# Kernel optimization log

Hardware: AMD Instinct MI355X
Metric: run time of the kernel (lower is better)

Reference implementation:

```python
import jax, jax.numpy as jnp
import numpy as np

E = 16          # num_expert
CAP = 1024


def setup_inputs() -> dict:
    key = jax.random.key(0)
    k1, k2, k3, k4 = jax.random.split(key, 4)
    B, L, D_in, D_out, S = 2, 4096, 1024, 4096, 512
    inp = jax.random.normal(k1, (B, L, D_in), jnp.float32)
    # counts must sum to B*L; use a balanced assignment (tokens pre-sorted by expert)
    fwd_expert_count = jnp.full((E,), (B * L) // E, dtype=jnp.int32)
    weight = jax.random.normal(k2, (E, D_out, D_in), jnp.float32) * (1.0 / np.sqrt(D_in))
    bias = jax.random.normal(k3, (E, D_out), jnp.float32) * 0.02
    components = jax.random.normal(k4, (E, S, D_out), jnp.float32) * (1.0 / np.sqrt(D_out))
    return {"inp": inp, "fwd_expert_count": fwd_expert_count, "weight": weight,
            "bias": bias, "components": components}


def _forward(inp, fwd_expert_count, weight, bias, components):
    flat = inp.reshape(-1, inp.shape[-1])            # [T, D_in]
    T = flat.shape[0]
    n_exp = fwd_expert_count.shape[0]
    counts = fwd_expert_count.astype(jnp.int32)
    # per-token expert id and position within its expert segment (tokens are
    # contiguous per expert, matching fastmoe's dispatch layout)
    expert_ids = jnp.repeat(jnp.arange(n_exp, dtype=jnp.int32), counts,
                            total_repeat_length=T)                    # [T]
    offsets = jnp.concatenate([jnp.zeros((1,), jnp.int32), jnp.cumsum(counts)])
    pos = jnp.arange(T, dtype=jnp.int32) - offsets[expert_ids]        # [T]
    # scatter tokens into a padded [E, CAP, D_in] buffer (static capacity)
    padded = jnp.zeros((n_exp, CAP, flat.shape[-1]), flat.dtype)
    padded = padded.at[expert_ids, pos].set(flat)
    # grouped expert GEMM: y_e = x_e @ W_e^T + b_e  (padded rows never read back)
    y = jnp.einsum('eci,eoi->eco', padded, weight) + bias[:, None, :]  # [E, CAP, D_out]
    # projection onto components (einsum 'nkd,ksd->nks' in padded layout)
    proj = jnp.einsum('ecd,esd->ecs', y, components)                   # [E, CAP, S]
    # gather real tokens back (the upscale_proj branch in the source is dead code:
    # its result is never used in the returned output)
    out = proj[expert_ids, pos]                                        # [T, S]
    return out.reshape(inp.shape[:-1] + (proj.shape[-1],))


def reference(inp, fwd_expert_count, weight, bias, components):
    return _forward(inp, fwd_expert_count, weight, bias, components)
```

## Files before the change

kernel.cpp:

```cpp
#include <hip/hip_runtime.h>


#define NEXP 16
#define TTOK 8192
#define DIN  1024
#define DOUT 4096
#define SDIM 512
#define LDSS 40

typedef short short8 __attribute__((ext_vector_type(8)));
typedef float floatx4 __attribute__((ext_vector_type(4)));
typedef unsigned short ushort_t;

__device__ __forceinline__ ushort_t f2bf(float f) {
    union { float f; unsigned u; } v; v.f = f;
    unsigned r = v.u + 0x7FFFu + ((v.u >> 16) & 1u);
    return (ushort_t)(r >> 16);
}

#define GLL16(g, l) __builtin_amdgcn_global_load_lds( \
    (const __attribute__((address_space(1))) void*)(g), \
    (__attribute__((address_space(3))) void*)(l), 16, 0, 0)

__global__ __launch_bounds__(256)
void cvt_kernel(const float* __restrict__ src, ushort_t* __restrict__ dst, int n8) {
    const int i = blockIdx.x * 256 + threadIdx.x;
    if (i >= n8) return;
    const float4 a = ((const float4*)src)[2 * i];
    const float4 b = ((const float4*)src)[2 * i + 1];
    short8 o;
    o[0] = (short)f2bf(a.x); o[1] = (short)f2bf(a.y);
    o[2] = (short)f2bf(a.z); o[3] = (short)f2bf(a.w);
    o[4] = (short)f2bf(b.x); o[5] = (short)f2bf(b.y);
    o[6] = (short)f2bf(b.z); o[7] = (short)f2bf(b.w);
    ((short8*)dst)[i] = o;
}

template<bool G1>
__global__ __launch_bounds__(512, 2)
void gemm8p(const ushort_t* __restrict__ Ain, const int* __restrict__ counts,
            const ushort_t* __restrict__ Bin, const float* __restrict__ bias,
            ushort_t* __restrict__ Yout, float* __restrict__ Pout) {
    __shared__ __align__(16) ushort_t As[2 * 16384];
    __shared__ __align__(16) ushort_t Bs[2 * 16384];

    int e, mt, nt, kq;
    if constexpr (G1) {
        const int l = ((blockIdx.x & 7) << 6) | (blockIdx.x >> 3);
        e = l >> 5; nt = (l >> 1) & 15; mt = l & 1; kq = 0;
    } else {
        const int l = ((blockIdx.x & 7) << 5) | (blockIdx.x >> 3);
        e = l >> 4; kq = (l >> 2) & 3; nt = (l >> 1) & 1; mt = l & 1;
    }
    const int LDK = G1 ? DIN : DOUT;

    int off = 0;
    for (int i = 0; i < e; ++i) off += counts[i];
    const int cnt = counts[e];

    const int tid = threadIdx.x, wave = tid >> 6, lane = tid & 63;
    const int wm = wave >> 2, wn = wave & 3;
    const int l15 = lane & 15, quad = lane >> 4;

    const int srow  = (wave << 3) + (lane >> 3);
    const int kbase = (G1 ? 0 : (kq << 10)) + (((lane & 7) ^ (lane >> 3)) << 3);

    const ushort_t* Bseg;
    if constexpr (G1) Bseg = Bin + (size_t)e * DOUT * DIN  + ((size_t)(nt << 8)) * DIN;
    else              Bseg = Bin + (size_t)e * SDIM * DOUT + ((size_t)(nt << 8)) * DOUT;
    const int aseg = off + (mt << 8);

    auto stA = [&](int bufe, int q, int kt) {
        int r = aseg + (q << 6) + srow; if (r >= TTOK) r = TTOK - 1;
        GLL16(Ain + (size_t)r * LDK + kbase + (kt << 6),
              As + bufe + (q << 12) + (wave << 9));
    };
    auto stB = [&](int bufe, int q, int kt) {
        GLL16(Bseg + (size_t)((q << 6) + srow) * LDK + kbase + (kt << 6),
              Bs + bufe + (q << 12) + (wave << 9));
    };
    auto rdA = [&](int bufe, int m, int s) -> short8 {
        return *(const short8*)&As[bufe + ((wm << 7) + (m << 4) + l15) * 64
                                   + ((((s << 2) | quad) ^ (lane & 7)) << 3)];
    };
    auto rdB = [&](int bufe, int n, int s) -> short8 {
        return *(const short8*)&Bs[bufe + ((wn << 6) + (n << 4) + l15) * 64
                                   + ((((s << 2) | quad) ^ (lane & 7)) << 3)];
    };

    floatx4 acc[8][4] = {};
    short8 bf[4][2], af0[2], af1[2];

#define RDB_ALL(BUFE) { _Pragma("unroll") \
    for (int n = 0; n < 4; ++n) { bf[n][0] = rdB(BUFE,n,0); bf[n][1] = rdB(BUFE,n,1); } }
#define RDA2(BUFE, M0) { af0[0]=rdA(BUFE,M0,0); af0[1]=rdA(BUFE,M0,1); \
                         af1[0]=rdA(BUFE,(M0)+1,0); af1[1]=rdA(BUFE,(M0)+1,1); }
#define MFMA16(M0) { \
    __builtin_amdgcn_s_setprio(1); \
    _Pragma("unroll") for (int n = 0; n < 4; ++n) { \
      acc[M0][n]     = __builtin_amdgcn_mfma_f32_16x16x32_bf16(af0[0], bf[n][0], acc[M0][n],     0,0,0); \
      acc[M0][n]     = __builtin_amdgcn_mfma_f32_16x16x32_bf16(af0[1], bf[n][1], acc[M0][n],     0,0,0); \
      acc[(M0)+1][n] = __builtin_amdgcn_mfma_f32_16x16x32_bf16(af1[0], bf[n][0], acc[(M0)+1][n], 0,0,0); \
      acc[(M0)+1][n] = __builtin_amdgcn_mfma_f32_16x16x32_bf16(af1[1], bf[n][1], acc[(M0)+1][n], 0,0,0); } \
    __builtin_amdgcn_s_setprio(0); }
#define BAR() __builtin_amdgcn_s_barrier()
#define VMC6() asm volatile("s_waitcnt vmcnt(6)" ::: "memory")

    stA(0,0,0); stA(0,1,0); stA(0,2,0); stA(0,3,0);
    stB(0,0,0); stB(0,1,0); stB(0,2,0); stB(0,3,0);
    stB(16384,0,1); stB(16384,1,1); stB(16384,2,1); stB(16384,3,1);
    stA(16384,0,1); stA(16384,2,1);
    VMC6();
    BAR();

    #pragma unroll 1
    for (int it = 0; it < 8; ++it) {
        const int tn = 2 * it + 1;
        const int t2 = (it < 7) ? 2 * it + 2 : 0;
        const int t3 = (it < 7) ? 2 * it + 3 : 1;

        RDB_ALL(0); RDA2(0, 0);
        stA(16384,1,tn); stA(16384,3,tn);
        BAR(); MFMA16(0); BAR();

        RDA2(0, 2);
        stB(0,0,t2); stB(0,1,t2);
        BAR(); MFMA16(2); BAR();

        RDA2(0, 4);
        stB(0,2,t2); stA(0,0,t2);
        BAR(); MFMA16(4); BAR();

        RDA2(0, 6);
        stB(0,3,t2); stA(0,2,t2);
        VMC6();
        BAR(); MFMA16(6); BAR();

        RDB_ALL(16384); RDA2(16384, 0);
        stA(0,1,t2); stA(0,3,t2);
        BAR(); MFMA16(0); BAR();

        RDA2(16384, 2);
        stB(16384,0,t3); stB(16384,1,t3);
        BAR(); MFMA16(2); BAR();

        RDA2(16384, 4);
        stB(16384,2,t3); stA(16384,0,t3);
        BAR(); MFMA16(4); BAR();

        RDA2(16384, 6);
        stB(16384,3,t3); stA(16384,2,t3);
        VMC6();
        BAR(); MFMA16(6); BAR();
    }
    asm volatile("s_waitcnt vmcnt(0)" ::: "memory");

#undef RDB_ALL
#undef RDA2
#undef MFMA16
#undef BAR
#undef VMC6

    if constexpr (G1) {
        float bv[4];
        #pragma unroll
        for (int n = 0; n < 4; ++n)
            bv[n] = bias[e * DOUT + (nt << 8) + (wn << 6) + (n << 4) + l15];
        #pragma unroll
        for (int m = 0; m < 8; ++m) {
            #pragma unroll
            for (int rg = 0; rg < 4; ++rg) {
                const int trow = (mt << 8) + (wm << 7) + (m << 4) + (quad << 2) + rg;
                if (trow < cnt) {
                    ushort_t* yp = Yout + (size_t)(off + trow) * DOUT + (nt << 8) + (wn << 6);
                    #pragma unroll
                    for (int n = 0; n < 4; ++n)
                        yp[(n << 4) + l15] = f2bf(acc[m][n][rg] + bv[n]);
                }
            }
        }
    } else {
        float* pp = Pout + (size_t)kq * ((size_t)TTOK * SDIM);
        #pragma unroll
        for (int m = 0; m < 8; ++m) {
            #pragma unroll
            for (int rg = 0; rg < 4; ++rg) {
                const int trow = (mt << 8) + (wm << 7) + (m << 4) + (quad << 2) + rg;
                if (trow < cnt) {
                    float* op = pp + (size_t)(off + trow) * SDIM + (nt << 8) + (wn << 6);
                    #pragma unroll
                    for (int n = 0; n < 4; ++n)
                        op[(n << 4) + l15] = acc[m][n][rg];
                }
            }
        }
    }
}

__global__ __launch_bounds__(256)
void reduce4_kernel(const float* __restrict__ P, float* __restrict__ O) {
    const int i = blockIdx.x * 256 + threadIdx.x;
    const size_t S = (size_t)TTOK * SDIM;
    const float4 a = ((const float4*)P)[i];
    const float4 b = ((const float4*)(P + S))[i];
    const float4 c = ((const float4*)(P + 2 * S))[i];
    const float4 d = ((const float4*)(P + 3 * S))[i];
    ((float4*)O)[i] = make_float4(a.x + b.x + c.x + d.x, a.y + b.y + c.y + d.y,
                                  a.z + b.z + c.z + d.z, a.w + b.w + c.w + d.w);
}

__global__ __launch_bounds__(256, 2)
void gemm1_o(const float* __restrict__ X, const int* __restrict__ counts,
             const float* __restrict__ W, const float* __restrict__ bias,
             ushort_t* __restrict__ Y) {
    __shared__ __align__(16) ushort_t As[128 * LDSS];
    __shared__ __align__(16) ushort_t Bs[128 * LDSS];
    const int bid = blockIdx.x;
    const int e = bid >> 7, r_ = bid & 127;
    const int n_tile = r_ >> 2, m_tile = r_ & 3;
    int off = 0;
    for (int i = 0; i < e; ++i) off += counts[i];
    const int cnt = counts[e];
    const int t = threadIdx.x, wave = t >> 6, lane = t & 63;
    const int wm = (wave & 1) << 6, wn = (wave >> 1) << 6;
    const int l15 = lane & 15, quad = lane >> 4;
    const float* Wp = W + (size_t)e * DOUT * DIN + (size_t)(n_tile << 7) * DIN;
    floatx4 acc[4][4] = {};
    const int srow = t >> 3, scol = (t & 7) << 2;
    for (int k0 = 0; k0 < DIN; k0 += 32) {
        #pragma unroll
        for (int p = 0; p < 4; ++p) {
            const int row = srow + (p << 5);
            int grow = off + (m_tile << 7) + row;
            if (grow >= TTOK) grow = 0;
            const float4 v = *(const float4*)(X + (size_t)grow * DIN + k0 + scol);
            unsigned lo = (unsigned)f2bf(v.x) | ((unsigned)f2bf(v.y) << 16);
            unsigned hi = (unsigned)f2bf(v.z) | ((unsigned)f2bf(v.w) << 16);
            *(uint2*)&As[row * LDSS + scol] = make_uint2(lo, hi);
        }
        #pragma unroll
        for (int p = 0; p < 4; ++p) {
            const int row = srow + (p << 5);
            const float4 v = *(const float4*)(Wp + (size_t)row * DIN + k0 + scol);
            unsigned lo = (unsigned)f2bf(v.x) | ((unsigned)f2bf(v.y) << 16);
            unsigned hi = (unsigned)f2bf(v.z) | ((unsigned)f2bf(v.w) << 16);
            *(uint2*)&Bs[row * LDSS + scol] = make_uint2(lo, hi);
        }
        __syncthreads();
        short8 af[4], bfr[4];
        #pragma unroll
        for (int i = 0; i < 4; ++i) {
            af[i]  = *(const short8*)&As[(wm + (i << 4) + l15) * LDSS + (quad << 3)];
            bfr[i] = *(const short8*)&Bs[(wn + (i << 4) + l15) * LDSS + (quad << 3)];
        }
        #pragma unroll
        for (int mi = 0; mi < 4; ++mi)
            #pragma unroll
            for (int ni = 0; ni < 4; ++ni)
                acc[mi][ni] = __builtin_amdgcn_mfma_f32_16x16x32_bf16(
                    af[mi], bfr[ni], acc[mi][ni], 0, 0, 0);
        __syncthreads();
    }
    float bv[4];
    #pragma unroll
    for (int ni = 0; ni < 4; ++ni)
        bv[ni] = bias[e * DOUT + (n_tile << 7) + wn + (ni << 4) + l15];
    #pragma unroll
    for (int mi = 0; mi < 4; ++mi)
        #pragma unroll
        for (int rg = 0; rg < 4; ++rg) {
            const int trow = (m_tile << 7) + wm + (mi << 4) + (quad << 2) + rg;
            if (trow < cnt) {
                ushort_t* yp = Y + (size_t)(off + trow) * DOUT + (n_tile << 7) + wn;
                #pragma unroll
                for (int ni = 0; ni < 4; ++ni)
                    yp[(ni << 4) + l15] = f2bf(acc[mi][ni][rg] + bv[ni]);
            }
        }
}

__global__ __launch_bounds__(256, 2)
void gemm2_o(const ushort_t* __restrict__ Y, const int* __restrict__ counts,
             const float* __restrict__ C, float* __restrict__ O) {
    __shared__ __align__(16) ushort_t As[128 * LDSS];
    __shared__ __align__(16) ushort_t Bs[128 * LDSS];
    const int bid = blockIdx.x;
    const int e = bid >> 4, r_ = bid & 15;
    const int n_tile = r_ >> 2, m_tile = r_ & 3;
    int off = 0;
    for (int i = 0; i < e; ++i) off += counts[i];
    const int cnt = counts[e];
    const int t = threadIdx.x, wave = t >> 6, lane = t & 63;
    const int wm = (wave & 1) << 6, wn = (wave >> 1) << 6;
    const int l15 = lane & 15, quad = lane >> 4;
    const float* Cp = C + (size_t)e * SDIM * DOUT + (size_t)(n_tile << 7) * DOUT;
    floatx4 acc[4][4] = {};
    const int arow = t >> 2, achk = (t & 3) << 3;
    const int srow = t >> 3, scol = (t & 7) << 2;
    for (int k0 = 0; k0 < DOUT; k0 += 32) {
        #pragma unroll
        for (int p = 0; p < 2; ++p) {
            const int row = arow + (p << 6);
            int grow = off + (m_tile << 7) + row;
            if (grow >= TTOK) grow = 0;
            const short8 v = *(const short8*)(Y + (size_t)grow * DOUT + k0 + achk);
            *(short8*)&As[row * LDSS + achk] = v;
        }
        #pragma unroll
        for (int p = 0; p < 4; ++p) {
            const int row = srow + (p << 5);
            const float4 v = *(const float4*)(Cp + (size_t)row * DOUT + k0 + scol);
            unsigned lo = (unsigned)f2bf(v.x) | ((unsigned)f2bf(v.y) << 16);
            unsigned hi = (unsigned)f2bf(v.z) | ((unsigned)f2bf(v.w) << 16);
            *(uint2*)&Bs[row * LDSS + scol] = make_uint2(lo, hi);
        }
        __syncthreads();
        short8 af[4], bfr[4];
        #pragma unroll
        for (int i = 0; i < 4; ++i) {
            af[i]  = *(const short8*)&As[(wm + (i << 4) + l15) * LDSS + (quad << 3)];
            bfr[i] = *(const short8*)&Bs[(wn + (i << 4) + l15) * LDSS + (quad << 3)];
        }
        #pragma unroll
        for (int mi = 0; mi < 4; ++mi)
            #pragma unroll
            for (int ni = 0; ni < 4; ++ni)
                acc[mi][ni] = __builtin_amdgcn_mfma_f32_16x16x32_bf16(
                    af[mi], bfr[ni], acc[mi][ni], 0, 0, 0);
        __syncthreads();
    }
    #pragma unroll
    for (int mi = 0; mi < 4; ++mi)
        #pragma unroll
        for (int rg = 0; rg < 4; ++rg) {
            const int trow = (m_tile << 7) + wm + (mi << 4) + (quad << 2) + rg;
            if (trow < cnt) {
                float* op = O + (size_t)(off + trow) * SDIM + (n_tile << 7) + wn;
                #pragma unroll
                for (int ni = 0; ni < 4; ++ni)
                    op[(ni << 4) + l15] = acc[mi][ni][rg];
            }
        }
}

extern "C" void kernel_launch(void* const* d_in, const int* in_sizes, int n_in,
                              void* d_out, int out_size, void* d_ws, size_t ws_size,
                              hipStream_t stream) {
    const float* X      = (const float*)d_in[0];
    const int*   counts = (const int*)d_in[1];
    const float* W      = (const float*)d_in[2];
    const float* bias   = (const float*)d_in[3];
    const float* comp   = (const float*)d_in[4];
    float* out = (float*)d_out;

    const size_t OFF_XB = 0;
    const size_t OFF_WB = 16777216;
    const size_t OFF_CB = 150994944;
    const size_t OFF_Y  = 218103808;
    const size_t NEED   = 285212672;

    if (ws_size >= NEED) {
        ushort_t* Xb = (ushort_t*)((char*)d_ws + OFF_XB);
        ushort_t* Wb = (ushort_t*)((char*)d_ws + OFF_WB);
        ushort_t* Cb = (ushort_t*)((char*)d_ws + OFF_CB);
        ushort_t* Y  = (ushort_t*)((char*)d_ws + OFF_Y);
        float*    P  = (float*)((char*)d_ws + OFF_WB);

        cvt_kernel<<<dim3(4096),  dim3(256), 0, stream>>>(X, Xb, 1048576);
        cvt_kernel<<<dim3(32768), dim3(256), 0, stream>>>(W, Wb, 8388608);
        cvt_kernel<<<dim3(16384), dim3(256), 0, stream>>>(comp, Cb, 4194304);
        gemm8p<true><<<dim3(512),  dim3(512), 0, stream>>>(Xb, counts, Wb, bias, Y, nullptr);
        gemm8p<false><<<dim3(256), dim3(512), 0, stream>>>(Y, counts, Cb, nullptr, nullptr, P);
        reduce4_kernel<<<dim3(4096), dim3(256), 0, stream>>>(P, out);
    } else {
        ushort_t* Y = (ushort_t*)d_ws;
        gemm1_o<<<dim3(2048), dim3(256), 0, stream>>>(X, counts, W, bias, Y);
        gemm2_o<<<dim3(256),  dim3(256), 0, stream>>>(Y, counts, comp, out);
    }
}
```

Measured before the change: 633.2 us.

## Fuse fp32-to-bf16 conversion of weights and components into GEMM B-tile loads

```diff
diff --git a/kernel.cpp b/kernel.cpp
--- a/kernel.cpp
+++ b/kernel.cpp
@@ -16,6 +16,12 @@
     union { float f; unsigned u; } v; v.f = f;
     unsigned r = v.u + 0x7FFFu + ((v.u >> 16) & 1u);
     return (ushort_t)(r >> 16);
+}
+
+__device__ __forceinline__ unsigned cvtpk(float lo, float hi) {
+    unsigned r;
+    asm("v_cvt_pk_bf16_f32 %0, %1, %2" : "=v"(r) : "v"(lo), "v"(hi));
+    return r;
 }
 
 #define GLL16(g, l) __builtin_amdgcn_global_load_lds( \
@@ -39,7 +45,7 @@
 template<bool G1>
 __global__ __launch_bounds__(512, 2)
 void gemm8p(const ushort_t* __restrict__ Ain, const int* __restrict__ counts,
-            const ushort_t* __restrict__ Bin, const float* __restrict__ bias,
+            const float* __restrict__ Bf, const float* __restrict__ bias,
             ushort_t* __restrict__ Yout, float* __restrict__ Pout) {
     __shared__ __align__(16) ushort_t As[2 * 16384];
     __shared__ __align__(16) ushort_t Bs[2 * 16384];
@@ -61,24 +67,28 @@
     const int tid = threadIdx.x, wave = tid >> 6, lane = tid & 63;
     const int wm = wave >> 2, wn = wave & 3;
     const int l15 = lane & 15, quad = lane >> 4;
-
-    const int srow  = (wave << 3) + (lane >> 3);
-    const int kbase = (G1 ? 0 : (kq << 10)) + (((lane & 7) ^ (lane >> 3)) << 3);
-
-    const ushort_t* Bseg;
-    if constexpr (G1) Bseg = Bin + (size_t)e * DOUT * DIN  + ((size_t)(nt << 8)) * DIN;
-    else              Bseg = Bin + (size_t)e * SDIM * DOUT + ((size_t)(nt << 8)) * DOUT;
+    const int srow = (wave << 3) + (lane >> 3);
+    const int swz8 = ((lane & 7) ^ (lane >> 3)) << 3;
     const int aseg = off + (mt << 8);
 
-    auto stA = [&](int bufe, int q, int kt) {
+    const ushort_t* ap[4];
+    #pragma unroll
+    for (int q = 0; q < 4; ++q) {
         int r = aseg + (q << 6) + srow; if (r >= TTOK) r = TTOK - 1;
-        GLL16(Ain + (size_t)r * LDK + kbase + (kt << 6),
-              As + bufe + (q << 12) + (wave << 9));
-    };
-    auto stB = [&](int bufe, int q, int kt) {
-        GLL16(Bseg + (size_t)((q << 6) + srow) * LDK + kbase + (kt << 6),
-              Bs + bufe + (q << 12) + (wave << 9));
-    };
+        ap[q] = Ain + (size_t)r * LDK + (G1 ? 0 : (kq << 10)) + swz8;
+    }
+    const float* bpq[4];
+    {
+        const float* Bbase = G1
+            ? (Bf + (size_t)e * DOUT * DIN  + ((size_t)(nt << 8)) * DIN)
+            : (Bf + (size_t)e * SDIM * DOUT + ((size_t)(nt << 8)) * DOUT + (kq << 10));
+        #pragma unroll
+        for (int q = 0; q < 4; ++q)
+            bpq[q] = Bbase + (size_t)((q << 6) + srow) * LDK + ((lane & 7) << 3);
+    }
+    const int aLdsW  = (wave << 9);
+    const int bWrOff = (srow << 6) + swz8;
+
     auto rdA = [&](int bufe, int m, int s) -> short8 {
         return *(const short8*)&As[bufe + ((wm << 7) + (m << 4) + l15) * 64
                                    + ((((s << 2) | quad) ^ (lane & 7)) << 3)];
@@ -89,77 +99,76 @@
     };
 
     floatx4 acc[8][4] = {};
-    short8 bf[4][2], af0[2], af1[2];
-
+    short8 bfv[4][2], af0[2], af1[2];
+    float4 bq[4][2];
+
+#define GA(NB, q, kt) GLL16(ap[q] + ((kt) << 6), As + (NB) + ((q) << 12) + aLdsW)
+#define LB(q, kt) { const float* _p = bpq[q] + ((kt) << 6); \
+    bq[q][0] = *(const float4*)_p; bq[q][1] = *(const float4*)(_p + 4); }
+#define WRB(NB, q) { uint4 _w; \
+    _w.x = cvtpk(bq[q][0].x, bq[q][0].y); _w.y = cvtpk(bq[q][0].z, bq[q][0].w); \
+    _w.z = cvtpk(bq[q][1].x, bq[q][1].y); _w.w = cvtpk(bq[q][1].z, bq[q][1].w); \
+    *(uint4*)&Bs[(NB) + ((q) << 12) + bWrOff] = _w; }
 #define RDB_ALL(BUFE) { _Pragma("unroll") \
-    for (int n = 0; n < 4; ++n) { bf[n][0] = rdB(BUFE,n,0); bf[n][1] = rdB(BUFE,n,1); } }
+    for (int n = 0; n < 4; ++n) { bfv[n][0] = rdB(BUFE,n,0); bfv[n][1] = rdB(BUFE,n,1); } }
 #define RDA2(BUFE, M0) { af0[0]=rdA(BUFE,M0,0); af0[1]=rdA(BUFE,M0,1); \
                          af1[0]=rdA(BUFE,(M0)+1,0); af1[1]=rdA(BUFE,(M0)+1,1); }
 #define MFMA16(M0) { \
     __builtin_amdgcn_s_setprio(1); \
     _Pragma("unroll") for (int n = 0; n < 4; ++n) { \
-      acc[M0][n]     = __builtin_amdgcn_mfma_f32_16x16x32_bf16(af0[0], bf[n][0], acc[M0][n],     0,0,0); \
-      acc[M0][n]     = __builtin_amdgcn_mfma_f32_16x16x32_bf16(af0[1], bf[n][1], acc[M0][n],     0,0,0); \
-      acc[(M0)+1][n] = __builtin_amdgcn_mfma_f32_16x16x32_bf16(af1[0], bf[n][0], acc[(M0)+1][n], 0,0,0); \
-      acc[(M0)+1][n] = __builtin_amdgcn_mfma_f32_16x16x32_bf16(af1[1], bf[n][1], acc[(M0)+1][n], 0,0,0); } \
+      acc[M0][n]     = __builtin_amdgcn_mfma_f32_16x16x32_bf16(af0[0], bfv[n][0], acc[M0][n],     0,0,0); \
+      acc[M0][n]     = __builtin_amdgcn_mfma_f32_16x16x32_bf16(af0[1], bfv[n][1], acc[M0][n],     0,0,0); \
+      acc[(M0)+1][n] = __builtin_amdgcn_mfma_f32_16x16x32_bf16(af1[0], bfv[n][0], acc[(M0)+1][n], 0,0,0); \
+      acc[(M0)+1][n] = __builtin_amdgcn_mfma_f32_16x16x32_bf16(af1[1], bfv[n][1], acc[(M0)+1][n], 0,0,0); } \
     __builtin_amdgcn_s_setprio(0); }
-#define BAR() __builtin_amdgcn_s_barrier()
-#define VMC6() asm volatile("s_waitcnt vmcnt(6)" ::: "memory")
-
-    stA(0,0,0); stA(0,1,0); stA(0,2,0); stA(0,3,0);
-    stB(0,0,0); stB(0,1,0); stB(0,2,0); stB(0,3,0);
-    stB(16384,0,1); stB(16384,1,1); stB(16384,2,1); stB(16384,3,1);
-    stA(16384,0,1); stA(16384,2,1);
-    VMC6();
-    BAR();
+#define VMC(N) asm volatile("s_waitcnt vmcnt(" #N ")" ::: "memory")
+#define LGKM0  asm volatile("s_waitcnt lgkmcnt(0)" ::: "memory")
+#define BAR()  __builtin_amdgcn_s_barrier()
+
+#define TILE(BUF, NBUF, KA, KB) { \
+    RDB_ALL(BUF); RDA2(BUF, 0); \
+    GA(NBUF, 0, KA); GA(NBUF, 1, KA); \
+    VMC(6); WRB(NBUF, 0); WRB(NBUF, 1); \
+    LGKM0; BAR(); MFMA16(0); BAR(); \
+    RDA2(BUF, 2); \
+    GA(NBUF, 2, KA); GA(NBUF, 3, KA); \
+    VMC(4); WRB(NBUF, 2); WRB(NBUF, 3); \
+    LGKM0; BAR(); MFMA16(2); BAR(); \
+    RDA2(BUF, 4); \
+    LB(0, KB); LB(1, KB); \
+    BAR(); MFMA16(4); BAR(); \
+    RDA2(BUF, 6); \
+    LB(2, KB); LB(3, KB); \
+    VMC(8); \
+    BAR(); MFMA16(6); BAR(); }
+
+    LB(0, 0); LB(1, 0); LB(2, 0); LB(3, 0);
+    GA(0, 0, 0); GA(0, 1, 0); GA(0, 2, 0); GA(0, 3, 0);
+    VMC(4);
+    WRB(0, 0); WRB(0, 1); WRB(0, 2); WRB(0, 3);
+    LB(0, 1); LB(1, 1); LB(2, 1); LB(3, 1);
+    VMC(8);
+    LGKM0; BAR();
 
     #pragma unroll 1
     for (int it = 0; it < 8; ++it) {
-        const int tn = 2 * it + 1;
-        const int t2 = (it < 7) ? 2 * it + 2 : 0;
-        const int t3 = (it < 7) ? 2 * it + 3 : 1;
-
-        RDB_ALL(0); RDA2(0, 0);
-        stA(16384,1,tn); stA(16384,3,tn);
-        BAR(); MFMA16(0); BAR();
-
-        RDA2(0, 2);
-        stB(0,0,t2); stB(0,1,t2);
-        BAR(); MFMA16(2); BAR();
-
-        RDA2(0, 4);
-        stB(0,2,t2); stA(0,0,t2);
-        BAR(); MFMA16(4); BAR();
-
-        RDA2(0, 6);
-        stB(0,3,t2); stA(0,2,t2);
-        VMC6();
-        BAR(); MFMA16(6); BAR();
-
-        RDB_ALL(16384); RDA2(16384, 0);
-        stA(0,1,t2); stA(0,3,t2);
-        BAR(); MFMA16(0); BAR();
-
-        RDA2(16384, 2);
-        stB(16384,0,t3); stB(16384,1,t3);
-        BAR(); MFMA16(2); BAR();
-
-        RDA2(16384, 4);
-        stB(16384,2,t3); stA(16384,0,t3);
-        BAR(); MFMA16(4); BAR();
-
-        RDA2(16384, 6);
-        stB(16384,3,t3); stA(16384,2,t3);
-        VMC6();
-        BAR(); MFMA16(6); BAR();
-    }
-    asm volatile("s_waitcnt vmcnt(0)" ::: "memory");
-
+        const int ka0 = 2 * it + 1;
+        const int kb0 = (it < 7) ? 2 * it + 2 : 15;
+        const int kb1 = (it < 7) ? 2 * it + 3 : 15;
+        TILE(0, 16384, ka0, kb0);
+        TILE(16384, 0, kb0, kb1);
+    }
+
+#undef TILE
+#undef GA
+#undef LB
+#undef WRB
 #undef RDB_ALL
 #undef RDA2
 #undef MFMA16
+#undef VMC
+#undef LGKM0
 #undef BAR
-#undef VMC6
 
     if constexpr (G1) {
         float bv[4];
@@ -354,23 +363,18 @@
     float* out = (float*)d_out;
 
     const size_t OFF_XB = 0;
-    const size_t OFF_WB = 16777216;
-    const size_t OFF_CB = 150994944;
-    const size_t OFF_Y  = 218103808;
-    const size_t NEED   = 285212672;
+    const size_t OFF_Y  = 16777216;
+    const size_t OFF_P  = 83886080;
+    const size_t NEED   = 150994944;
 
     if (ws_size >= NEED) {
         ushort_t* Xb = (ushort_t*)((char*)d_ws + OFF_XB);
-        ushort_t* Wb = (ushort_t*)((char*)d_ws + OFF_WB);
-        ushort_t* Cb = (ushort_t*)((char*)d_ws + OFF_CB);
         ushort_t* Y  = (ushort_t*)((char*)d_ws + OFF_Y);
-        float*    P  = (float*)((char*)d_ws + OFF_WB);
-
-        cvt_kernel<<<dim3(4096),  dim3(256), 0, stream>>>(X, Xb, 1048576);
-        cvt_kernel<<<dim3(32768), dim3(256), 0, stream>>>(W, Wb, 8388608);
-        cvt_kernel<<<dim3(16384), dim3(256), 0, stream>>>(comp, Cb, 4194304);
-        gemm8p<true><<<dim3(512),  dim3(512), 0, stream>>>(Xb, counts, Wb, bias, Y, nullptr);
-        gemm8p<false><<<dim3(256), dim3(512), 0, stream>>>(Y, counts, Cb, nullptr, nullptr, P);
+        float*    P  = (float*)((char*)d_ws + OFF_P);
+
+        cvt_kernel<<<dim3(4096), dim3(256), 0, stream>>>(X, Xb, 1048576);
+        gemm8p<true><<<dim3(512),  dim3(512), 0, stream>>>(Xb, counts, W, bias, Y, nullptr);
+        gemm8p<false><<<dim3(256), dim3(512), 0, stream>>>(Y, counts, comp, nullptr, nullptr, P);
         reduce4_kernel<<<dim3(4096), dim3(256), 0, stream>>>(P, out);
     } else {
         ushort_t* Y = (ushort_t*)d_ws;
```

After: 566.3 us. -10.6%, faster.
